# Kernel optimization log

Measured on AMD Instinct MI355X. Metric: run time of the kernel, lower is better.

The kernel has to match this reference:

```python
import jax, jax.numpy as jnp
import numpy as np

B, T, D, H, L, DFF, MAXLEN = 4, 2048, 512, 8, 6, 2048, 2048
DK = D // H
SCALE = float(1.0 / np.sqrt(DK * 2))  # 1/sqrt(d_k*2)


def layer_norm(x, g, b, eps=1e-5):
    m = jnp.mean(x, axis=-1, keepdims=True)
    v = jnp.var(x, axis=-1, keepdims=True)
    return (x - m) / jnp.sqrt(v + eps) * g + b


def setup_inputs() -> dict:
    key = jax.random.key(0)
    it = iter(jax.random.split(key, 48))
    def n(shape, std=0.02):
        return jax.random.normal(next(it), shape, dtype=jnp.float32) * std
    inp = {}
    inp['x'] = jax.random.normal(next(it), (B, T), dtype=jnp.float32)
    inp['ip_w'] = n((1, D)); inp['ip_b'] = jnp.zeros((D,))
    inp['ip_ln_g'] = jnp.ones((D,)); inp['ip_ln_b'] = jnp.zeros((D,))
    inp['pos_embed'] = n((MAXLEN, D), 0.01)
    inp['pad_token'] = n((D,), 0.01)
    inp['Wq'] = n((L, D, D)); inp['bq'] = jnp.zeros((L, D))
    inp['Wk'] = n((L, D, D)); inp['bk'] = jnp.zeros((L, D))
    inp['Wv'] = n((L, D, D)); inp['bv'] = jnp.zeros((L, D))
    inp['Wo'] = n((L, D, D)); inp['bo'] = jnp.zeros((L, D))
    inp['ln1_g'] = jnp.ones((L, D)); inp['ln1_b'] = jnp.zeros((L, D))
    inp['ln2_g'] = jnp.ones((L, D)); inp['ln2_b'] = jnp.zeros((L, D))
    inp['W1'] = n((L, D, DFF)); inp['b1'] = jnp.zeros((L, DFF))
    inp['W2'] = n((L, DFF, D)); inp['b2'] = jnp.zeros((L, D))
    inp['gate1'] = jnp.full((L,), 0.1); inp['gate2'] = jnp.full((L,), 0.1)
    inp['fn_g'] = jnp.ones((D,)); inp['fn_b'] = jnp.zeros((D,))
    for p in ['bh', 'ah', 'ch']:
        inp[p + '_ln_g'] = jnp.ones((D,)); inp[p + '_ln_b'] = jnp.zeros((D,))
    inp['bh_w'] = n((D, 2), 0.01); inp['bh_b'] = jnp.zeros((2,))
    inp['ah_w'] = n((D, 1), 0.01); inp['ah_b'] = jnp.zeros((1,))
    inp['ch_w'] = n((D, 1), 0.01); inp['ch_b'] = jnp.zeros((1,))
    return inp


def _forward(x, ip_w, ip_b, ip_ln_g, ip_ln_b, pos_embed, pad_token,
             Wq, bq, Wk, bk, Wv, bv, Wo, bo,
             ln1_g, ln1_b, ln2_g, ln2_b, W1, b1, W2, b2, gate1, gate2,
             fn_g, fn_b, bh_ln_g, bh_ln_b, bh_w, bh_b,
             ah_ln_g, ah_ln_b, ah_w, ah_b, ch_ln_g, ch_ln_b, ch_w, ch_b):
    Bx, Tx = x.shape
    xc = jnp.clip(x, -10.0, 10.0)
    pad_mask = xc == -1.0  # [B,T]
    h = layer_norm(xc[..., None] @ ip_w + ip_b, ip_ln_g, ip_ln_b)  # [B,T,D]
    h = h + 0.1 * pos_embed[None, :Tx, :]
    h = jnp.where(pad_mask[..., None], pad_token, h)
    cmask = jnp.triu(jnp.full((Tx, Tx), -10000.0, dtype=h.dtype), k=1)  # additive causal mask
    for i in range(L):
        xn = layer_norm(h, ln1_g[i], ln1_b[i])
        def heads(w, b, xn=xn):
            return (xn @ w + b).reshape(Bx, Tx, H, DK).transpose(0, 2, 1, 3)
        q = heads(Wq[i], bq[i]); k = heads(Wk[i], bk[i]); v = heads(Wv[i], bv[i])
        q = q / jnp.maximum(jnp.linalg.norm(q, axis=-1, keepdims=True), 1e-8)
        k = k / jnp.maximum(jnp.linalg.norm(k, axis=-1, keepdims=True), 1e-8)
        scores = jnp.clip(jnp.einsum('bhtd,bhsd->bhts', q, k) * SCALE, -5.0, 5.0) + cmask
        a = jax.nn.softmax(scores / 1.5, axis=-1)
        o = jnp.einsum('bhts,bhsd->bhtd', a, v).transpose(0, 2, 1, 3).reshape(Bx, Tx, D)
        h = h + gate1[i] * ((o @ Wo[i] + bo[i]) * 0.5)
        xn2 = layer_norm(h, ln2_g[i], ln2_b[i])
        ffn = jax.nn.gelu(xn2 @ W1[i] + b1[i], approximate=False) @ W2[i] + b2[i]
        h = jnp.clip(h + gate2[i] * ffn, -10.0, 10.0)
    h = layer_norm(h, fn_g, fn_b)
    m = (~pad_mask).astype(h.dtype)[..., None]
    mean = (h * m).sum(axis=1) / jnp.maximum(m.sum(axis=1), 1.0)  # masked mean pool [B,D]
    binary = layer_norm(mean, bh_ln_g, bh_ln_b) @ bh_w + bh_b
    anomaly = layer_norm(mean, ah_ln_g, ah_ln_b) @ ah_w + ah_b
    caustic = jax.nn.sigmoid(layer_norm(mean, ch_ln_g, ch_ln_b) @ ch_w + ch_b)
    return jnp.concatenate([binary, anomaly, caustic], axis=-1)  # [B,4]


def reference(x, ip_w, ip_b, ip_ln_g, ip_ln_b, pos_embed, pad_token,
              Wq, bq, Wk, bk, Wv, bv, Wo, bo,
              ln1_g, ln1_b, ln2_g, ln2_b, W1, b1, W2, b2, gate1, gate2,
              fn_g, fn_b, bh_ln_g, bh_ln_b, bh_w, bh_b,
              ah_ln_g, ah_ln_b, ah_w, ah_b, ch_ln_g, ch_ln_b, ch_w, ch_b):
    return _forward(x, ip_w, ip_b, ip_ln_g, ip_ln_b, pos_embed, pad_token,
                    Wq, bq, Wk, bk, Wv, bv, Wo, bo,
                    ln1_g, ln1_b, ln2_g, ln2_b, W1, b1, W2, b2, gate1, gate2,
                    fn_g, fn_b, bh_ln_g, bh_ln_b, bh_w, bh_b,
                    ah_ln_g, ah_ln_b, ah_w, ah_b, ch_ln_g, ch_ln_b, ch_w, ch_b)
```

## Files before the change

kernel.cpp:

```cpp
#include <hip/hip_runtime.h>
#include <hip/hip_bf16.h>
#include <math.h>

constexpr int Bsz = 4, T = 2048, D = 512, H = 8, Lnum = 6, DFF = 2048, DK = 64;
constexpr int QS2 = 1024;
constexpr float K2 = 0.08838834764831845f / 1.5f;

typedef __attribute__((ext_vector_type(8))) short svec8;
typedef __attribute__((ext_vector_type(4))) float fvec4;

__device__ __forceinline__ fvec4 mfma16(svec8 a, svec8 b, fvec4 c) {
    return __builtin_amdgcn_mfma_f32_16x16x32_bf16(a, b, c, 0, 0, 0);
}
__device__ __forceinline__ unsigned short f2b(float f) {
    unsigned int u = __float_as_uint(f);
    u += 0x7fffu + ((u >> 16) & 1u);
    return (unsigned short)(u >> 16);
}
__device__ __forceinline__ unsigned int pk2b(float a, float b) {
    __hip_bfloat162 h = __float22bfloat162_rn(float2{a, b});
    return *(unsigned int*)&h;
}
__device__ __forceinline__ float wave_red_sum(float v) {
    for (int o = 32; o > 0; o >>= 1) v += __shfl_down(v, o, 64);
    return __shfl(v, 0, 64);
}
__device__ __forceinline__ void glds16(const unsigned short* g, unsigned short* l) {
    __builtin_amdgcn_global_load_lds(
        (const __attribute__((address_space(1))) unsigned int*)g,
        (__attribute__((address_space(3))) unsigned int*)l, 16, 0, 0);
}
#define FRAG(buf, row, kq) (*(const svec8*)((buf) + (((row) << 6) | ((((kq) ^ ((row) & 7))) << 3))))

__global__ __launch_bounds__(64)
void embed_kernel(const float* __restrict__ x, const float* __restrict__ ip_w,
                  const float* __restrict__ ip_b, const float* __restrict__ g,
                  const float* __restrict__ bta, const float* __restrict__ pos,
                  const float* __restrict__ pad_tok, float* __restrict__ h)
{
    int row = blockIdx.x;
    int t = row & (T - 1);
    int lane = threadIdx.x;
    float xv = x[row];
    float xc = fminf(fmaxf(xv, -10.f), 10.f);
    bool pad = (xc == -1.0f);
    float pre[8];
    float s = 0.f, s2 = 0.f;
#pragma unroll
    for (int j = 0; j < 8; j++) {
        int d = j * 64 + lane;
        float p = xc * ip_w[d] + ip_b[d];
        pre[j] = p; s += p; s2 += p * p;
    }
    s = wave_red_sum(s); s2 = wave_red_sum(s2);
    float m = s * (1.f / 512.f);
    float var = s2 * (1.f / 512.f) - m * m;
    float rstd = 1.f / sqrtf(var + 1e-5f);
#pragma unroll
    for (int j = 0; j < 8; j++) {
        int d = j * 64 + lane;
        float hv = (pre[j] - m) * rstd * g[d] + bta[d] + 0.1f * pos[(size_t)t * D + d];
        if (pad) hv = pad_tok[d];
        h[(size_t)row * D + d] = hv;
    }
}

__global__ __launch_bounds__(256)
void ln_kernel(const float* __restrict__ in, float* __restrict__ out,
               const float* __restrict__ g, const float* __restrict__ b)
{
    int row = blockIdx.x * 4 + (threadIdx.x >> 6);
    int lane = threadIdx.x & 63;
    const float* r = in + (size_t)row * D;
    float4 v0 = ((const float4*)r)[lane];
    float4 v1 = ((const float4*)r)[lane + 64];
    float s = v0.x + v0.y + v0.z + v0.w + v1.x + v1.y + v1.z + v1.w;
    float s2 = v0.x*v0.x + v0.y*v0.y + v0.z*v0.z + v0.w*v0.w
             + v1.x*v1.x + v1.y*v1.y + v1.z*v1.z + v1.w*v1.w;
    s = wave_red_sum(s); s2 = wave_red_sum(s2);
    float m = s * (1.f / 512.f);
    float var = s2 * (1.f / 512.f) - m * m;
    float rstd = 1.f / sqrtf(var + 1e-5f);
    float4 g0 = ((const float4*)g)[lane], g1 = ((const float4*)g)[lane + 64];
    float4 b0 = ((const float4*)b)[lane], b1 = ((const float4*)b)[lane + 64];
    float4 o0, o1;
    o0.x = (v0.x - m) * rstd * g0.x + b0.x; o0.y = (v0.y - m) * rstd * g0.y + b0.y;
    o0.z = (v0.z - m) * rstd * g0.z + b0.z; o0.w = (v0.w - m) * rstd * g0.w + b0.w;
    o1.x = (v1.x - m) * rstd * g1.x + b1.x; o1.y = (v1.y - m) * rstd * g1.y + b1.y;
    o1.z = (v1.z - m) * rstd * g1.z + b1.z; o1.w = (v1.w - m) * rstd * g1.w + b1.w;
    ((float4*)(out + (size_t)row * D))[lane] = o0;
    ((float4*)(out + (size_t)row * D))[lane + 64] = o1;
}

__device__ __forceinline__ void ln_row_bf16(const float* __restrict__ in, unsigned short* __restrict__ out,
                                            const float* __restrict__ g, const float* __restrict__ b,
                                            int row, int lane)
{
    const float* r = in + (size_t)row * D;
    float4 v0 = ((const float4*)r)[lane];
    float4 v1 = ((const float4*)r)[lane + 64];
    float s = v0.x + v0.y + v0.z + v0.w + v1.x + v1.y + v1.z + v1.w;
    float s2 = v0.x*v0.x + v0.y*v0.y + v0.z*v0.z + v0.w*v0.w
             + v1.x*v1.x + v1.y*v1.y + v1.z*v1.z + v1.w*v1.w;
    s = wave_red_sum(s); s2 = wave_red_sum(s2);
    float m = s * (1.f / 512.f);
    float var = s2 * (1.f / 512.f) - m * m;
    float rstd = 1.f / sqrtf(var + 1e-5f);
    float4 g0 = ((const float4*)g)[lane], g1 = ((const float4*)g)[lane + 64];
    float4 b0 = ((const float4*)b)[lane], b1 = ((const float4*)b)[lane + 64];
    unsigned short o0[4], o1[4];
    o0[0] = f2b((v0.x - m) * rstd * g0.x + b0.x); o0[1] = f2b((v0.y - m) * rstd * g0.y + b0.y);
    o0[2] = f2b((v0.z - m) * rstd * g0.z + b0.z); o0[3] = f2b((v0.w - m) * rstd * g0.w + b0.w);
    o1[0] = f2b((v1.x - m) * rstd * g1.x + b1.x); o1[1] = f2b((v1.y - m) * rstd * g1.y + b1.y);
    o1[2] = f2b((v1.z - m) * rstd * g1.z + b1.z); o1[3] = f2b((v1.w - m) * rstd * g1.w + b1.w);
    *(uint2*)(out + (size_t)row * D + lane * 4) = *(uint2*)o0;
    *(uint2*)(out + (size_t)row * D + 256 + lane * 4) = *(uint2*)o1;
}

__global__ __launch_bounds__(256)
void ln_bf16_kernel(const float* __restrict__ in, unsigned short* __restrict__ out,
                    const float* __restrict__ g, const float* __restrict__ b)
{
    ln_row_bf16(in, out, g, b, blockIdx.x * 4 + (threadIdx.x >> 6), threadIdx.x & 63);
}

__global__ __launch_bounds__(256)
void prep_kernel(const float* __restrict__ wq, const float* __restrict__ wk,
                 const float* __restrict__ wv, const float* __restrict__ wo,
                 const float* __restrict__ w1, const float* __restrict__ w2,
                 unsigned short* __restrict__ oq, unsigned short* __restrict__ ok,
                 unsigned short* __restrict__ ov, unsigned short* __restrict__ oo,
                 unsigned short* __restrict__ o1, unsigned short* __restrict__ o2,
                 const float* __restrict__ hin, unsigned short* __restrict__ lnout,
                 const float* __restrict__ ln_g, const float* __restrict__ ln_b)
{
    __shared__ float tile[32][33];
    int bid = blockIdx.x;
    if (bid >= 3072) {
        int row = (bid - 3072) * 4 + (threadIdx.x >> 6);
        ln_row_bf16(hin, lnout, ln_g, ln_b, row, threadIdx.x & 63);
        return;
    }
    const float* in; unsigned short* out; int K, N, kt, nt;
    if (bid < 1024) {
        int sel = bid >> 8, loc = bid & 255;
        in  = sel == 0 ? wq : sel == 1 ? wk : sel == 2 ? wv : wo;
        out = sel == 0 ? oq : sel == 1 ? ok : sel == 2 ? ov : oo;
        K = 512; N = 512; kt = loc >> 4; nt = loc & 15;
    } else if (bid < 2048) {
        int loc = bid - 1024; in = w1; out = o1; K = 512; N = 2048; kt = loc >> 6; nt = loc & 63;
    } else {
        int loc = bid - 2048; in = w2; out = o2; K = 2048; N = 512; kt = loc >> 4; nt = loc & 15;
    }
    int k0 = kt * 32, n0 = nt * 32;
    int t = threadIdx.x;
    int kr = t >> 3, nc = (t & 7) * 4;
    float4 v = *(const float4*)(in + (size_t)(k0 + kr) * N + n0 + nc);
    tile[kr][nc] = v.x; tile[kr][nc + 1] = v.y; tile[kr][nc + 2] = v.z; tile[kr][nc + 3] = v.w;
    __syncthreads();
    unsigned short o[4];
#pragma unroll
    for (int i = 0; i < 4; i++) o[i] = f2b(tile[nc + i][kr]);
    *(uint2*)(out + (size_t)(n0 + kr) * K + k0 + nc) = *(uint2*)o;
}

template<int EPI, int OBF, int BM>
__global__ __launch_bounds__(256)
void gemm_bf16(const unsigned short* __restrict__ A, const unsigned short* __restrict__ BT,
               const float* __restrict__ bias, const float* __restrict__ bias_b,
               const float* __restrict__ bias_c, const float* __restrict__ res,
               void* __restrict__ Cv, unsigned short* __restrict__ vtout,
               int M, int N, int K, const float* __restrict__ gate_p)
{
    constexpr int WN = (BM == 128) ? 2 : 4;
    constexpr int WSPAN = 128 / WN;
    constexpr int NT = WSPAN / 16;
    constexpr int MT = 4;
    constexpr int ACALLS = BM / 32;
    constexpr int SMEMSZ = (EPI == 0) ? 17408 : (BM * 64 + 128 * 64);
    __shared__ __align__(16) unsigned short SMEM[SMEMSZ];
    unsigned short* As = SMEM;
    unsigned short* Bs = SMEM + BM * 64;
    const int tid = threadIdx.x, w = tid >> 6, lane = tid & 63, quad = lane >> 4, ln = lane & 15;
    const int wm = w / WN, wn = w % WN;
    const int m0 = blockIdx.x * BM, n0 = blockIdx.y * 128;
    const int jg = (lane & 7) ^ ((lane >> 3) & 7);
    const int rb = w * 8 + (lane >> 3);
    const unsigned short* Agl = A + (size_t)(m0 + rb) * K + jg * 8;
    const unsigned short* Bgl = BT + (size_t)(n0 + rb) * K + jg * 8;

    fvec4 acc[MT][NT];
#pragma unroll
    for (int mt = 0; mt < MT; mt++)
#pragma unroll
        for (int nt = 0; nt < NT; nt++)
#pragma unroll
            for (int r = 0; r < 4; r++) acc[mt][nt][r] = 0.f;

    for (int k0 = 0; k0 < K; k0 += 64) {
        __syncthreads();
#pragma unroll
        for (int c = 0; c < ACALLS; c++)
            glds16(Agl + k0 + (size_t)c * 32 * K, As + c * 2048 + w * 512);
#pragma unroll
        for (int c = 0; c < 4; c++)
            glds16(Bgl + k0 + (size_t)c * 32 * K, Bs + c * 2048 + w * 512);
        __syncthreads();
#pragma unroll
        for (int kk = 0; kk < 2; kk++) {
            svec8 af[MT], bfr[NT];
#pragma unroll
            for (int mt = 0; mt < MT; mt++)
                af[mt] = FRAG(As, wm * 64 + mt * 16 + ln, kk * 4 + quad);
#pragma unroll
            for (int nt = 0; nt < NT; nt++)
                bfr[nt] = FRAG(Bs, wn * WSPAN + nt * 16 + ln, kk * 4 + quad);
#pragma unroll
            for (int mt = 0; mt < MT; mt++)
#pragma unroll
                for (int nt = 0; nt < NT; nt++)
                    acc[mt][nt] = mfma16(af[mt], bfr[nt], acc[mt][nt]);
        }
    }

    const float gate = (EPI == 1 || EPI == 3) ? gate_p[0] : 0.f;
    float bb[NT];
#pragma unroll
    for (int nt = 0; nt < NT; nt++) {
        int n = n0 + wn * WSPAN + nt * 16 + ln;
        if (EPI == 0) {
            int nseg = n >> 9;
            const float* bsel = nseg == 0 ? bias : (nseg == 1 ? bias_b : bias_c);
            bb[nt] = bsel[n - nseg * 512];
        } else {
            bb[nt] = bias[n];
        }
    }

    if (EPI == 0 && n0 >= 1024) {
        __syncthreads();
#pragma unroll
        for (int mt = 0; mt < MT; mt++) {
#pragma unroll
            for (int nt = 0; nt < NT; nt++) {
                int nl = wn * 64 + nt * 16 + ln;
                int mb = wm * 64 + mt * 16 + quad * 4;
                unsigned int lo = pk2b(acc[mt][nt][0] + bb[nt], acc[mt][nt][1] + bb[nt]);
                unsigned int hi = pk2b(acc[mt][nt][2] + bb[nt], acc[mt][nt][3] + bb[nt]);
                uint2 u; u.x = lo; u.y = hi;
                *(uint2*)(SMEM + nl * 136 + mb) = u;
            }
        }
        __syncthreads();
        int row = tid >> 1, half = (tid & 1) * 64;
        unsigned short* dst = vtout + ((size_t)((m0 >> 11) * 512 + (n0 - 1024) + row)) * T
                              + (m0 & (T - 1)) + half;
        const unsigned short* src = SMEM + row * 136 + half;
#pragma unroll
        for (int j = 0; j < 8; j++) *(uint4*)(dst + j * 8) = *(const uint4*)(src + j * 8);
        return;
    }

#pragma unroll
    for (int mt = 0; mt < MT; mt++) {
        float v[NT][4];
#pragma unroll
        for (int nt = 0; nt < NT; nt++)
#pragma unroll
            for (int r = 0; r < 4; r++) v[nt][r] = acc[mt][nt][r] + bb[nt];
        if (EPI == 0) {
            const float fac = ((n0 + wn * WSPAN) < 512) ? K2 : 1.f;
#pragma unroll
            for (int r = 0; r < 4; r++) {
                float s = 0.f;
#pragma unroll
                for (int nt = 0; nt < NT; nt++) s += v[nt][r] * v[nt][r];
                s += __shfl_xor(s, 1); s += __shfl_xor(s, 2);
                s += __shfl_xor(s, 4); s += __shfl_xor(s, 8);
                float rs = fac / fmaxf(sqrtf(s), 1e-8f);
#pragma unroll
                for (int nt = 0; nt < NT; nt++) v[nt][r] *= rs;
            }
        }
#pragma unroll
        for (int nt = 0; nt < NT; nt++) {
            int n = n0 + wn * WSPAN + nt * 16 + ln;
#pragma unroll
            for (int r = 0; r < 4; r++) {
                int m = m0 + wm * 64 + mt * 16 + quad * 4 + r;
                float val = v[nt][r];
                if (EPI == 0) {
                    ((unsigned short*)Cv)[(size_t)m * QS2 + n] = f2b(val);
                } else {
                    size_t off = (size_t)m * N + n;
                    if (EPI == 1) val = res[off] + gate * 0.5f * val;
                    else if (EPI == 2) {
                        float u = val;
                        float z = 0.7978845608028654f * fmaf(0.044715f * u, u * u, u);
                        float e = __builtin_amdgcn_exp2f(z * 2.8853900817779268f);
                        float rr = __builtin_amdgcn_rcpf(e + 1.f);
                        val = u * (1.f - rr);
                    }
                    else if (EPI == 3) val = fminf(fmaxf(res[off] + gate * val, -10.f), 10.f);
                    if (OBF) ((unsigned short*)Cv)[off] = f2b(val);
                    else ((float*)Cv)[off] = val;
                }
            }
        }
    }
}

template<bool DIAG>
__device__ __forceinline__ void attn_step32(
    unsigned short* Ps, const unsigned short* Ks, const unsigned short* Vt,
    const svec8 (&qf)[2][2], fvec4 (&oacc)[2][4], fvec4 (&lacc)[2],
    int w, int quad, int ln)
{
    constexpr short BONE = (short)0x3F80;
    const svec8 ONES8 = {BONE, BONE, BONE, BONE, BONE, BONE, BONE, BONE};
#pragma unroll
    for (int nt = 0; nt < 4; nt++) {
        svec8 kf0 = FRAG(Ks, nt * 16 + ln, quad);
        svec8 kf1 = FRAG(Ks, nt * 16 + ln, 4 + quad);
        const int sbase = nt * 16 + quad * 4;
#pragma unroll
        for (int qg = 0; qg < 2; qg++) {
            fvec4 z; z[0] = z[1] = z[2] = z[3] = 0.f;
            z = mfma16(kf0, qf[qg][0], z);
            z = mfma16(kf1, qf[qg][1], z);
            const int qcol = w * 32 + qg * 16 + ln;
            float p[4];
#pragma unroll
            for (int r = 0; r < 4; r++) {
                float y = z[r];
                float pv = fmaf(y, fmaf(y, 0.5f, 1.f), 1.f);
                if (DIAG && (sbase + r > qcol)) pv = 0.f;
                p[r] = pv;
            }
            uint2 u; u.x = pk2b(p[0], p[1]); u.y = pk2b(p[2], p[3]);
            const int paddr = (qcol << 6) | ((((sbase >> 3) ^ (qcol & 7))) << 3) | (sbase & 7);
            *(uint2*)(Ps + paddr) = u;
        }
    }
#pragma unroll
    for (int ks = 0; ks < 2; ks++) {
        svec8 pa[2];
#pragma unroll
        for (int qg = 0; qg < 2; qg++) {
            pa[qg] = FRAG(Ps, w * 32 + qg * 16 + ln, ks * 4 + quad);
            lacc[qg] = mfma16(pa[qg], ONES8, lacc[qg]);
        }
#pragma unroll
        for (int dkn = 0; dkn < 4; dkn++) {
            svec8 vf = FRAG(Vt, dkn * 16 + ln, ks * 4 + quad);
#pragma unroll
            for (int qg = 0; qg < 2; qg++)
                oacc[qg][dkn] = mfma16(pa[qg], vf, oacc[qg][dkn]);
        }
    }
}

__global__ __launch_bounds__(128)
void attn_kernel(const unsigned short* __restrict__ qkv, const unsigned short* __restrict__ vt,
                 unsigned short* __restrict__ o)
{
    __shared__ __align__(16) unsigned short K0[4096], V0[4096], K1[4096], V1[4096];
    __shared__ __align__(16) unsigned short Ps[4096];
    const int fid = blockIdx.x;
    const int c = fid & 255, slot = fid >> 8, k = c >> 5;
    const int bh = c & 31;
    const int qt = (slot == 0) ? k : (slot == 1) ? 15 - k : (slot == 2) ? 16 + k : 31 - k;
    const int b = bh >> 3, hh = bh & 7;
    const int nst = qt + 1;
    const int tid = threadIdx.x, w = tid >> 6, lane = tid & 63, quad = lane >> 4, ln = lane & 15;
    const int jgz = (lane & 7) ^ (lane >> 3);

    svec8 qf[2][2];
#pragma unroll
    for (int qg = 0; qg < 2; qg++) {
        const unsigned short* qp = qkv + ((size_t)(b * T + qt * 64 + w * 32 + qg * 16 + ln)) * QS2 + hh * 64;
        qf[qg][0] = *(const svec8*)(qp + quad * 8);
        qf[qg][1] = *(const svec8*)(qp + 32 + quad * 8);
    }

    const unsigned short* kbase = qkv + ((size_t)(b * T) + w * 8 + (lane >> 3)) * QS2 + 512 + hh * 64 + jgz * 8;
    const unsigned short* vbase = vt + ((size_t)(bh * 64) + w * 8 + (lane >> 3)) * T + jgz * 8;
    const int ldsoff = w * 8 * 64;

    fvec4 oacc[2][4], lacc[2];
#pragma unroll
    for (int qg = 0; qg < 2; qg++) {
#pragma unroll
        for (int r = 0; r < 4; r++) lacc[qg][r] = 0.f;
#pragma unroll
        for (int dkn = 0; dkn < 4; dkn++)
#pragma unroll
            for (int r = 0; r < 4; r++) oacc[qg][dkn][r] = 0.f;
    }

    const int Nph = (nst + 1) >> 1;
    for (int ph = 0; ph < Nph; ph++) {
        const int s0 = 2 * ph, s1 = 2 * ph + 1;
        __syncthreads();
#pragma unroll
        for (int cc = 0; cc < 4; cc++) {
            glds16(kbase + ((size_t)(s0 * 64) + cc * 16) * QS2, K0 + cc * 1024 + ldsoff);
            glds16(vbase + (size_t)(cc * 16) * T + s0 * 64, V0 + cc * 1024 + ldsoff);
        }
        if (s1 < nst) {
#pragma unroll
            for (int cc = 0; cc < 4; cc++) {
                glds16(kbase + ((size_t)(s1 * 64) + cc * 16) * QS2, K1 + cc * 1024 + ldsoff);
                glds16(vbase + (size_t)(cc * 16) * T + s1 * 64, V1 + cc * 1024 + ldsoff);
            }
        }
        __syncthreads();
        if (s0 == qt) attn_step32<true >(Ps, K0, V0, qf, oacc, lacc, w, quad, ln);
        else          attn_step32<false>(Ps, K0, V0, qf, oacc, lacc, w, quad, ln);
        if (s1 < nst) {
            if (s1 == qt) attn_step32<true >(Ps, K1, V1, qf, oacc, lacc, w, quad, ln);
            else          attn_step32<false>(Ps, K1, V1, qf, oacc, lacc, w, quad, ln);
        }
    }

    unsigned short* og = o + (size_t)(b * T + qt * 64 + w * 32 + quad * 4) * D + hh * 64;
#pragma unroll
    for (int qg = 0; qg < 2; qg++) {
#pragma unroll
        for (int r = 0; r < 4; r++) {
            float inv = 1.f / lacc[qg][r];
#pragma unroll
            for (int dkn = 0; dkn < 4; dkn++)
                og[(size_t)(qg * 16 + r) * D + dkn * 16 + ln] = f2b(oacc[qg][dkn][r] * inv);
        }
    }
}

__global__ __launch_bounds__(256)
void pool_kernel(const float* __restrict__ hn, const float* __restrict__ x, float* __restrict__ part)
{
    int b = blockIdx.x, ch = blockIdx.y, tid = threadIdx.x;
    int t0 = ch * 128;
    float s0 = 0.f, s1 = 0.f, cnt = 0.f;
    for (int tt = 0; tt < 128; tt++) {
        int t = t0 + tt;
        float xv = x[b * T + t];
        float m = (xv == -1.0f) ? 0.f : 1.f;
        cnt += m;
        const float* r = hn + ((size_t)(b * T + t)) * D;
        s0 += r[tid] * m;
        s1 += r[tid + 256] * m;
    }
    float* pr = part + (size_t)(b * 16 + ch) * 513;
    pr[tid] = s0; pr[tid + 256] = s1;
    if (tid == 0) pr[512] = cnt;
}

__global__ __launch_bounds__(64)
void head_kernel(const float* __restrict__ part,
                 const float* __restrict__ bh_g, const float* __restrict__ bh_bl,
                 const float* __restrict__ ah_g, const float* __restrict__ ah_bl,
                 const float* __restrict__ ch_g, const float* __restrict__ ch_bl,
                 const float* __restrict__ bh_w, const float* __restrict__ bh_b2,
                 const float* __restrict__ ah_w, const float* __restrict__ ah_b2,
                 const float* __restrict__ ch_w, const float* __restrict__ ch_b2,
                 float* __restrict__ out)
{
    int b = blockIdx.x, lane = threadIdx.x;
    float cnt = 0.f;
    for (int c = 0; c < 16; c++) cnt += part[(size_t)(b * 16 + c) * 513 + 512];
    float denom = fmaxf(cnt, 1.f);
    float md[8];
    float s = 0.f, s2 = 0.f;
#pragma unroll
    for (int j = 0; j < 8; j++) {
        int d = j * 64 + lane;
        float acc = 0.f;
        for (int c = 0; c < 16; c++) acc += part[(size_t)(b * 16 + c) * 513 + d];
        md[j] = acc / denom;
        s += md[j]; s2 += md[j] * md[j];
    }
    s = wave_red_sum(s); s2 = wave_red_sum(s2);
    float mu = s * (1.f / 512.f);
    float var = s2 * (1.f / 512.f) - mu * mu;
    float rstd = 1.f / sqrtf(var + 1e-5f);
    float a0 = 0.f, a1 = 0.f, a2 = 0.f, a3 = 0.f;
#pragma unroll
    for (int j = 0; j < 8; j++) {
        int d = j * 64 + lane;
        float z = (md[j] - mu) * rstd;
        float zb = z * bh_g[d] + bh_bl[d];
        a0 += zb * bh_w[d * 2 + 0];
        a1 += zb * bh_w[d * 2 + 1];
        a2 += (z * ah_g[d] + ah_bl[d]) * ah_w[d];
        a3 += (z * ch_g[d] + ch_bl[d]) * ch_w[d];
    }
    a0 = wave_red_sum(a0); a1 = wave_red_sum(a1);
    a2 = wave_red_sum(a2); a3 = wave_red_sum(a3);
    if (lane == 0) {
        out[b * 4 + 0] = a0 + bh_b2[0];
        out[b * 4 + 1] = a1 + bh_b2[1];
        out[b * 4 + 2] = a2 + ah_b2[0];
        float t3 = a3 + ch_b2[0];
        out[b * 4 + 3] = 1.f / (1.f + expf(-t3));
    }
}

extern "C" void kernel_launch(void* const* d_in, const int* in_sizes, int n_in,
                              void* d_out, int out_size, void* d_ws, size_t ws_size,
                              hipStream_t stream)
{
    const float* x      = (const float*)d_in[0];
    const float* ip_w   = (const float*)d_in[1];
    const float* ip_b   = (const float*)d_in[2];
    const float* ip_ln_g= (const float*)d_in[3];
    const float* ip_ln_b= (const float*)d_in[4];
    const float* pos    = (const float*)d_in[5];
    const float* pad_tok= (const float*)d_in[6];
    const float* Wq = (const float*)d_in[7];  const float* bq = (const float*)d_in[8];
    const float* Wk = (const float*)d_in[9];  const float* bk = (const float*)d_in[10];
    const float* Wv = (const float*)d_in[11]; const float* bv = (const float*)d_in[12];
    const float* Wo = (const float*)d_in[13]; const float* bo = (const float*)d_in[14];
    const float* ln1_g = (const float*)d_in[15]; const float* ln1_b = (const float*)d_in[16];
    const float* ln2_g = (const float*)d_in[17]; const float* ln2_b = (const float*)d_in[18];
    const float* W1 = (const float*)d_in[19]; const float* b1 = (const float*)d_in[20];
    const float* W2 = (const float*)d_in[21]; const float* b2 = (const float*)d_in[22];
    const float* gate1 = (const float*)d_in[23]; const float* gate2 = (const float*)d_in[24];
    const float* fn_g = (const float*)d_in[25]; const float* fn_b = (const float*)d_in[26];
    const float* bh_g  = (const float*)d_in[27]; const float* bh_bl = (const float*)d_in[28];
    const float* ah_g  = (const float*)d_in[29]; const float* ah_bl = (const float*)d_in[30];
    const float* ch_g  = (const float*)d_in[31]; const float* ch_bl = (const float*)d_in[32];
    const float* bh_w  = (const float*)d_in[33]; const float* bh_b2 = (const float*)d_in[34];
    const float* ah_w  = (const float*)d_in[35]; const float* ah_b2 = (const float*)d_in[36];
    const float* ch_w  = (const float*)d_in[37]; const float* ch_b2 = (const float*)d_in[38];

    char* ws = (char*)d_ws;
    float*          h     = (float*)ws;
    unsigned short* act_b = (unsigned short*)(ws + 16777216);
    unsigned short* qkv   = (unsigned short*)(ws + 25165824);
    unsigned short* mid_b = (unsigned short*)(ws + 41943040);
    float*          xn_f  = (float*)(ws + 41943040);
    unsigned short* wT    = (unsigned short*)(ws + 75497472);
    unsigned short* vt    = (unsigned short*)(ws + 81788928);
    float*          part  = (float*)(ws + 90177536);
    float*          out   = (float*)d_out;

    unsigned short* wqT = wT;
    unsigned short* wkT = wT + 262144;
    unsigned short* wvT = wT + 524288;
    unsigned short* woT = wT + 786432;
    unsigned short* w1T = wT + 1048576;
    unsigned short* w2T = wT + 2097152;

    embed_kernel<<<dim3(Bsz * T), dim3(64), 0, stream>>>(x, ip_w, ip_b, ip_ln_g, ip_ln_b, pos, pad_tok, h);

    for (int i = 0; i < Lnum; i++) {
        const size_t dd = (size_t)i * D * D;
        const size_t df = (size_t)i * D * DFF;
        prep_kernel<<<dim3(5120), dim3(256), 0, stream>>>(Wq + dd, Wk + dd, Wv + dd, Wo + dd,
                                                          W1 + df, W2 + df,
                                                          wqT, wkT, wvT, woT, w1T, w2T,
                                                          h, act_b, ln1_g + i * D, ln1_b + i * D);
        gemm_bf16<0, 1, 128><<<dim3(64, 12), dim3(256), 0, stream>>>(act_b, wqT, bq + i * D, bk + i * D, bv + i * D,
                                                                     nullptr, qkv, vt, Bsz * T, 1536, D, nullptr);
        attn_kernel<<<dim3(1024), dim3(128), 0, stream>>>(qkv, vt, act_b);
        gemm_bf16<1, 0, 64><<<dim3(128, 4), dim3(256), 0, stream>>>(act_b, woT, bo + i * D, nullptr, nullptr,
                                                                    h, h, nullptr, Bsz * T, D, D, gate1 + i);
        ln_bf16_kernel<<<dim3(Bsz * T / 4), dim3(256), 0, stream>>>(h, act_b, ln2_g + i * D, ln2_b + i * D);
        gemm_bf16<2, 1, 128><<<dim3(64, 16), dim3(256), 0, stream>>>(act_b, w1T, b1 + i * DFF, nullptr, nullptr,
                                                                     nullptr, mid_b, nullptr, Bsz * T, DFF, D, nullptr);
        gemm_bf16<3, 0, 64><<<dim3(128, 4), dim3(256), 0, stream>>>(mid_b, w2T, b2 + i * D, nullptr, nullptr,
                                                                    h, h, nullptr, Bsz * T, D, DFF, gate2 + i);
    }

    ln_kernel<<<dim3(Bsz * T / 4), dim3(256), 0, stream>>>(h, xn_f, fn_g, fn_b);
    pool_kernel<<<dim3(Bsz, 16), dim3(256), 0, stream>>>(xn_f, x, part);
    head_kernel<<<dim3(Bsz), dim3(64), 0, stream>>>(part, bh_g, bh_bl, ah_g, ah_bl, ch_g, ch_bl,
                                                    bh_w, bh_b2, ah_w, ah_b2, ch_w, ch_b2, out);
}
```

Measured before the change: 1.182 ms.

## Pair complementary causal query tiles per attention block to share K/V loads

```diff
diff --git a/kernel.cpp b/kernel.cpp
--- a/kernel.cpp
+++ b/kernel.cpp
@@ -310,10 +310,12 @@
     }
 }
 
-template<bool DIAG>
-__device__ __forceinline__ void attn_step32(
-    unsigned short* Ps, const unsigned short* Ks, const unsigned short* Vt,
-    const svec8 (&qf)[2][2], fvec4 (&oacc)[2][4], fvec4 (&lacc)[2],
+template<bool MA, bool DIAG>
+__device__ __forceinline__ void attn_stepP(
+    unsigned short* PsA, unsigned short* PsB,
+    const unsigned short* Ks, const unsigned short* Vt,
+    const svec8 (&qfA)[2][2], const svec8 (&qfB)[2][2],
+    fvec4 (&oA)[2][4], fvec4 (&lA)[2], fvec4 (&oB)[2][4], fvec4 (&lB)[2],
     int w, int quad, int ln)
 {
     constexpr short BONE = (short)0x3F80;
@@ -325,37 +327,60 @@
         const int sbase = nt * 16 + quad * 4;
 #pragma unroll
         for (int qg = 0; qg < 2; qg++) {
-            fvec4 z; z[0] = z[1] = z[2] = z[3] = 0.f;
-            z = mfma16(kf0, qf[qg][0], z);
-            z = mfma16(kf1, qf[qg][1], z);
             const int qcol = w * 32 + qg * 16 + ln;
-            float p[4];
-#pragma unroll
-            for (int r = 0; r < 4; r++) {
-                float y = z[r];
-                float pv = fmaf(y, fmaf(y, 0.5f, 1.f), 1.f);
-                if (DIAG && (sbase + r > qcol)) pv = 0.f;
-                p[r] = pv;
-            }
-            uint2 u; u.x = pk2b(p[0], p[1]); u.y = pk2b(p[2], p[3]);
             const int paddr = (qcol << 6) | ((((sbase >> 3) ^ (qcol & 7))) << 3) | (sbase & 7);
-            *(uint2*)(Ps + paddr) = u;
+            {
+                fvec4 z; z[0] = z[1] = z[2] = z[3] = 0.f;
+                z = mfma16(kf0, qfB[qg][0], z);
+                z = mfma16(kf1, qfB[qg][1], z);
+                float p[4];
+#pragma unroll
+                for (int r = 0; r < 4; r++) {
+                    float y = z[r];
+                    float pv = fmaf(y, fmaf(y, 0.5f, 1.f), 1.f);
+                    if (DIAG && !MA && (sbase + r > qcol)) pv = 0.f;
+                    p[r] = pv;
+                }
+                uint2 u; u.x = pk2b(p[0], p[1]); u.y = pk2b(p[2], p[3]);
+                *(uint2*)(PsB + paddr) = u;
+            }
+            if (MA) {
+                fvec4 z; z[0] = z[1] = z[2] = z[3] = 0.f;
+                z = mfma16(kf0, qfA[qg][0], z);
+                z = mfma16(kf1, qfA[qg][1], z);
+                float p[4];
+#pragma unroll
+                for (int r = 0; r < 4; r++) {
+                    float y = z[r];
+                    float pv = fmaf(y, fmaf(y, 0.5f, 1.f), 1.f);
+                    if (DIAG && (sbase + r > qcol)) pv = 0.f;
+                    p[r] = pv;
+                }
+                uint2 u; u.x = pk2b(p[0], p[1]); u.y = pk2b(p[2], p[3]);
+                *(uint2*)(PsA + paddr) = u;
+            }
         }
     }
 #pragma unroll
     for (int ks = 0; ks < 2; ks++) {
-        svec8 pa[2];
+        svec8 paB[2], paA[2];
 #pragma unroll
         for (int qg = 0; qg < 2; qg++) {
-            pa[qg] = FRAG(Ps, w * 32 + qg * 16 + ln, ks * 4 + quad);
-            lacc[qg] = mfma16(pa[qg], ONES8, lacc[qg]);
+            paB[qg] = FRAG(PsB, w * 32 + qg * 16 + ln, ks * 4 + quad);
+            lB[qg] = mfma16(paB[qg], ONES8, lB[qg]);
+            if (MA) {
+                paA[qg] = FRAG(PsA, w * 32 + qg * 16 + ln, ks * 4 + quad);
+                lA[qg] = mfma16(paA[qg], ONES8, lA[qg]);
+            }
         }
 #pragma unroll
         for (int dkn = 0; dkn < 4; dkn++) {
             svec8 vf = FRAG(Vt, dkn * 16 + ln, ks * 4 + quad);
 #pragma unroll
-            for (int qg = 0; qg < 2; qg++)
-                oacc[qg][dkn] = mfma16(pa[qg], vf, oacc[qg][dkn]);
+            for (int qg = 0; qg < 2; qg++) {
+                oB[qg][dkn] = mfma16(paB[qg], vf, oB[qg][dkn]);
+                if (MA) oA[qg][dkn] = mfma16(paA[qg], vf, oA[qg][dkn]);
+            }
         }
     }
 }
@@ -365,37 +390,40 @@
                  unsigned short* __restrict__ o)
 {
     __shared__ __align__(16) unsigned short K0[4096], V0[4096], K1[4096], V1[4096];
-    __shared__ __align__(16) unsigned short Ps[4096];
+    __shared__ __align__(16) unsigned short PsA[4096], PsB[4096];
     const int fid = blockIdx.x;
-    const int c = fid & 255, slot = fid >> 8, k = c >> 5;
-    const int bh = c & 31;
-    const int qt = (slot == 0) ? k : (slot == 1) ? 15 - k : (slot == 2) ? 16 + k : 31 - k;
+    const int xcd = fid & 7, slot = fid >> 3;
+    const int bh = xcd * 4 + (slot & 3);
+    const int p = slot >> 2;
     const int b = bh >> 3, hh = bh & 7;
-    const int nst = qt + 1;
+    const int qtA = p, qtB = 31 - p, nst = 32 - p;
     const int tid = threadIdx.x, w = tid >> 6, lane = tid & 63, quad = lane >> 4, ln = lane & 15;
     const int jgz = (lane & 7) ^ (lane >> 3);
 
-    svec8 qf[2][2];
+    svec8 qfA[2][2], qfB[2][2];
 #pragma unroll
     for (int qg = 0; qg < 2; qg++) {
-        const unsigned short* qp = qkv + ((size_t)(b * T + qt * 64 + w * 32 + qg * 16 + ln)) * QS2 + hh * 64;
-        qf[qg][0] = *(const svec8*)(qp + quad * 8);
-        qf[qg][1] = *(const svec8*)(qp + 32 + quad * 8);
+        const unsigned short* qpA = qkv + ((size_t)(b * T + qtA * 64 + w * 32 + qg * 16 + ln)) * QS2 + hh * 64;
+        const unsigned short* qpB = qkv + ((size_t)(b * T + qtB * 64 + w * 32 + qg * 16 + ln)) * QS2 + hh * 64;
+        qfA[qg][0] = *(const svec8*)(qpA + quad * 8);
+        qfA[qg][1] = *(const svec8*)(qpA + 32 + quad * 8);
+        qfB[qg][0] = *(const svec8*)(qpB + quad * 8);
+        qfB[qg][1] = *(const svec8*)(qpB + 32 + quad * 8);
     }
 
     const unsigned short* kbase = qkv + ((size_t)(b * T) + w * 8 + (lane >> 3)) * QS2 + 512 + hh * 64 + jgz * 8;
     const unsigned short* vbase = vt + ((size_t)(bh * 64) + w * 8 + (lane >> 3)) * T + jgz * 8;
     const int ldsoff = w * 8 * 64;
 
-    fvec4 oacc[2][4], lacc[2];
+    fvec4 oA[2][4], oB[2][4], lA[2], lB[2];
 #pragma unroll
     for (int qg = 0; qg < 2; qg++) {
 #pragma unroll
-        for (int r = 0; r < 4; r++) lacc[qg][r] = 0.f;
+        for (int r = 0; r < 4; r++) { lA[qg][r] = 0.f; lB[qg][r] = 0.f; }
 #pragma unroll
         for (int dkn = 0; dkn < 4; dkn++)
 #pragma unroll
-            for (int r = 0; r < 4; r++) oacc[qg][dkn][r] = 0.f;
+            for (int r = 0; r < 4; r++) { oA[qg][dkn][r] = 0.f; oB[qg][dkn][r] = 0.f; }
     }
 
     const int Nph = (nst + 1) >> 1;
@@ -415,23 +443,39 @@
             }
         }
         __syncthreads();
-        if (s0 == qt) attn_step32<true >(Ps, K0, V0, qf, oacc, lacc, w, quad, ln);
-        else          attn_step32<false>(Ps, K0, V0, qf, oacc, lacc, w, quad, ln);
+        {
+            if (s0 <= p) {
+                if (s0 == p) attn_stepP<true , true >(PsA, PsB, K0, V0, qfA, qfB, oA, lA, oB, lB, w, quad, ln);
+                else         attn_stepP<true , false>(PsA, PsB, K0, V0, qfA, qfB, oA, lA, oB, lB, w, quad, ln);
+            } else {
+                if (s0 == nst - 1) attn_stepP<false, true >(PsA, PsB, K0, V0, qfA, qfB, oA, lA, oB, lB, w, quad, ln);
+                else               attn_stepP<false, false>(PsA, PsB, K0, V0, qfA, qfB, oA, lA, oB, lB, w, quad, ln);
+            }
+        }
         if (s1 < nst) {
-            if (s1 == qt) attn_step32<true >(Ps, K1, V1, qf, oacc, lacc, w, quad, ln);
-            else          attn_step32<false>(Ps, K1, V1, qf, oacc, lacc, w, quad, ln);
-        }
-    }
-
-    unsigned short* og = o + (size_t)(b * T + qt * 64 + w * 32 + quad * 4) * D + hh * 64;
+            if (s1 <= p) {
+                if (s1 == p) attn_stepP<true , true >(PsA, PsB, K1, V1, qfA, qfB, oA, lA, oB, lB, w, quad, ln);
+                else         attn_stepP<true , false>(PsA, PsB, K1, V1, qfA, qfB, oA, lA, oB, lB, w, quad, ln);
+            } else {
+                if (s1 == nst - 1) attn_stepP<false, true >(PsA, PsB, K1, V1, qfA, qfB, oA, lA, oB, lB, w, quad, ln);
+                else               attn_stepP<false, false>(PsA, PsB, K1, V1, qfA, qfB, oA, lA, oB, lB, w, quad, ln);
+            }
+        }
+    }
+
+    unsigned short* ogA = o + (size_t)(b * T + qtA * 64 + w * 32 + quad * 4) * D + hh * 64;
+    unsigned short* ogB = o + (size_t)(b * T + qtB * 64 + w * 32 + quad * 4) * D + hh * 64;
 #pragma unroll
     for (int qg = 0; qg < 2; qg++) {
 #pragma unroll
         for (int r = 0; r < 4; r++) {
-            float inv = 1.f / lacc[qg][r];
-#pragma unroll
-            for (int dkn = 0; dkn < 4; dkn++)
-                og[(size_t)(qg * 16 + r) * D + dkn * 16 + ln] = f2b(oacc[qg][dkn][r] * inv);
+            float ia = 1.f / lA[qg][r];
+            float ib = 1.f / lB[qg][r];
+#pragma unroll
+            for (int dkn = 0; dkn < 4; dkn++) {
+                ogA[(size_t)(qg * 16 + r) * D + dkn * 16 + ln] = f2b(oA[qg][dkn][r] * ia);
+                ogB[(size_t)(qg * 16 + r) * D + dkn * 16 + ln] = f2b(oB[qg][dkn][r] * ib);
+            }
         }
     }
 }
@@ -563,7 +607,7 @@
                                                           h, act_b, ln1_g + i * D, ln1_b + i * D);
         gemm_bf16<0, 1, 128><<<dim3(64, 12), dim3(256), 0, stream>>>(act_b, wqT, bq + i * D, bk + i * D, bv + i * D,
                                                                      nullptr, qkv, vt, Bsz * T, 1536, D, nullptr);
-        attn_kernel<<<dim3(1024), dim3(128), 0, stream>>>(qkv, vt, act_b);
+        attn_kernel<<<dim3(512), dim3(128), 0, stream>>>(qkv, vt, act_b);
         gemm_bf16<1, 0, 64><<<dim3(128, 4), dim3(256), 0, stream>>>(act_b, woT, bo + i * D, nullptr, nullptr,
                                                                     h, h, nullptr, Bsz * T, D, D, gate1 + i);
         ln_bf16_kernel<<<dim3(Bsz * T / 4), dim3(256), 0, stream>>>(h, act_b, ln2_g + i * D, ln2_b + i * D);
```

Result: no change. 1.179 ms (-0.3%).
